# Kernel tuning notes

Measured on AMD Instinct MI355X. Metric: run time of the kernel, lower is better.

The kernel has to match this reference:

```python
import jax, jax.numpy as jnp
import numpy as np

N_NODES = 100000
N_EDGES = 1000000
NHID = 128
N_CLASSES = 5000


def setup_inputs() -> dict:
    key = jax.random.key(0)
    ks = jax.random.split(key, 8)
    feature = jax.random.normal(ks[0], (N_NODES, NHID), dtype=jnp.float32)
    # Linear weights stored as [in, out] so forward is x @ W + b
    W1 = jax.random.normal(ks[1], (2 * NHID, NHID), dtype=jnp.float32) * (1.0 / np.sqrt(2 * NHID))
    b1 = jnp.zeros((NHID,), dtype=jnp.float32)
    alpha = jnp.full((NHID,), 0.25, dtype=jnp.float32)  # PReLU per-channel init
    W2 = jax.random.normal(ks[2], (NHID, 2), dtype=jnp.float32) * (1.0 / np.sqrt(NHID))
    b2 = jnp.zeros((2,), dtype=jnp.float32)
    row = jax.random.randint(ks[3], (N_EDGES,), 0, N_NODES, dtype=jnp.int64)
    col = jax.random.randint(ks[4], (N_EDGES,), 0, N_NODES, dtype=jnp.int64)
    label = jax.random.randint(ks[5], (N_NODES,), 0, N_CLASSES, dtype=jnp.int64)
    return {"feature": feature, "W1": W1, "b1": b1, "alpha": alpha,
            "W2": W2, "b2": b2, "row": row, "col": col, "label": label}


def reference(feature, W1, b1, alpha, W2, b2, row, col, label):
    # per-edge label: 1 if endpoints share a cluster label
    y = (label[row] == label[col]).astype(jnp.int32)  # [E]
    # edge gather + concat: [E, 2*nhid]
    x = jnp.concatenate([feature[row], feature[col]], axis=1)
    h = x @ W1 + b1                                   # [E, nhid]
    h = jnp.where(h >= 0, h, alpha * h)               # PReLU, per-channel alpha
    logits = h @ W2 + b2                              # [E, 2]
    logp = jax.nn.log_softmax(logits, axis=-1)
    # mean cross-entropy over edges
    loss = -jnp.mean(jnp.take_along_axis(logp, y[:, None], axis=1))
    return loss
```

## Files before the change

### kernel.cpp

```cpp
#include <hip/hip_runtime.h>
#include <hip/hip_bf16.h>

typedef __bf16 bf16_t;
typedef bf16_t bf16x8 __attribute__((ext_vector_type(8)));
typedef float floatx4 __attribute__((ext_vector_type(4)));
typedef float floatx2 __attribute__((ext_vector_type(2)));

#define N_NODES 100000
#define N_EDGES 1000000
#define N_TILES 6250


__global__ __launch_bounds__(256) void k_prep(const float* __restrict__ W1,
                                              const float* __restrict__ b1,
                                              const float* __restrict__ alpha,
                                              const float* __restrict__ W2,
                                              const float* __restrict__ b2,
                                              bf16_t* __restrict__ WT,
                                              float* __restrict__ wabsp,
                                              float* __restrict__ u1g,
                                              float* __restrict__ u2g,
                                              float* __restrict__ constg,
                                              float* __restrict__ out) {
    __shared__ float w1L[128];
    int i = blockIdx.x * 256 + threadIdx.x;
    if (i < 32768) {
        int n = i >> 7;
        int k = i & 127;
        float v = (n < 128) ? W1[k * 128 + n] : W1[(k + 128) * 128 + (n - 128)];
        WT[i] = (bf16_t)v;
    }
    if (blockIdx.x == 128) {
        int t = threadIdx.x;
        if (t < 128) {
            float wd = W2[2 * t + 1] - W2[2 * t];
            float al = alpha[t];
            w1L[t] = wd * (1.f + al) * 0.5f;
            int c = (t & 7) * 16 + (t >> 3);
            float wdc = W2[2 * c + 1] - W2[2 * c];
            wabsp[t] = wdc * (1.f - alpha[c]) * 0.5f;
        }
        __syncthreads();
        if (t < 128) {
            float a1 = 0.f, a2 = 0.f;
            for (int j = 0; j < 128; ++j) {
                a1 = fmaf(W1[t * 128 + j], w1L[j], a1);
                a2 = fmaf(W1[(t + 128) * 128 + j], w1L[j], a2);
            }
            u1g[t] = a1;
            u2g[t] = a2;
        }
        if (t == 128) {
            float c = 0.f;
            for (int j = 0; j < 128; ++j) c = fmaf(w1L[j], b1[j], c);
            *constg = c + (b2[1] - b2[0]);
        }
        if (t == 129) out[0] = 0.f;
    }
}

__global__ __launch_bounds__(256) void k_gemm(const float* __restrict__ F,
                                              const bf16_t* __restrict__ WT,
                                              const float* __restrict__ b1,
                                              const float* __restrict__ u1g,
                                              const float* __restrict__ u2g,
                                              const int* __restrict__ label,
                                              unsigned char* __restrict__ PQ8,
                                              float4* __restrict__ aux_g) {
    const int w = threadIdx.x >> 6, lane = threadIdx.x & 63;
    const int l15 = lane & 15, quad = lane >> 4;
    const int h = w >> 1, jb = (w & 1) * 4;

    bf16x8 Bf[4][4];
    const bf16_t* wbase = WT + (size_t)(w * 64 + l15) * 128 + quad * 8;
#pragma unroll
    for (int s = 0; s < 4; ++s)
#pragma unroll
        for (int nt = 0; nt < 4; ++nt)
            Bf[s][nt] = *(const bf16x8*)(wbase + (size_t)nt * 2048 + s * 32);

    float bv[4];
#pragma unroll
    for (int nt = 0; nt < 4; ++nt)
        bv[nt] = (h == 0) ? b1[(jb + nt) * 16 + l15] : 0.f;

    for (int tile = blockIdx.x; tile < N_TILES; tile += gridDim.x) {
        const int m0 = tile * 16;
        const float4* Ar = (const float4*)(F + (size_t)(m0 + l15) * 128 + quad * 8);
        float4 fa[4], fb[4];
#pragma unroll
        for (int s = 0; s < 4; ++s) { fa[s] = Ar[s * 8]; fb[s] = Ar[s * 8 + 1]; }

        bf16x8 Af[4];
#pragma unroll
        for (int s = 0; s < 4; ++s) {
            bf16x8 v;
            v[0] = (bf16_t)fa[s].x; v[1] = (bf16_t)fa[s].y;
            v[2] = (bf16_t)fa[s].z; v[3] = (bf16_t)fa[s].w;
            v[4] = (bf16_t)fb[s].x; v[5] = (bf16_t)fb[s].y;
            v[6] = (bf16_t)fb[s].z; v[7] = (bf16_t)fb[s].w;
            Af[s] = v;
        }

        floatx4 acc[4] = {};
#pragma unroll
        for (int s = 0; s < 4; ++s)
#pragma unroll
            for (int nt = 0; nt < 4; ++nt)
                acc[nt] = __builtin_amdgcn_mfma_f32_16x16x32_bf16(Af[s], Bf[s][nt], acc[nt], 0, 0, 0);

        if (w == 0) {
            float s1 = 0.f, s2 = 0.f;
#pragma unroll
            for (int s = 0; s < 4; ++s) {
                const float* u1p = u1g + s * 32 + quad * 8;
                const float* u2p = u2g + s * 32 + quad * 8;
                float fv[8] = {fa[s].x, fa[s].y, fa[s].z, fa[s].w,
                               fb[s].x, fb[s].y, fb[s].z, fb[s].w};
#pragma unroll
                for (int j = 0; j < 8; ++j) {
                    s1 = fmaf(fv[j], u1p[j], s1);
                    s2 = fmaf(fv[j], u2p[j], s2);
                }
            }
            s1 += __shfl_xor(s1, 16, 64); s1 += __shfl_xor(s1, 32, 64);
            s2 += __shfl_xor(s2, 16, 64); s2 += __shfl_xor(s2, 32, 64);
            if (quad == 0) {
                int grow = m0 + l15;
                float4 av = {s1, s2, __int_as_float(label[grow]), 0.f};
                aux_g[grow] = av;
            }
        }

#pragma unroll
        for (int r = 0; r < 4; ++r) {
            int grow = m0 + quad * 4 + r;
            unsigned int pk = 0;
            pk = __builtin_amdgcn_cvt_pk_fp8_f32(acc[0][r] + bv[0], acc[1][r] + bv[1], pk, false);
            pk = __builtin_amdgcn_cvt_pk_fp8_f32(acc[2][r] + bv[2], acc[3][r] + bv[3], pk, true);
            *(unsigned int*)(PQ8 + (size_t)grow * 256 + h * 128 + l15 * 8 + jb) = pk;
        }
    }
}

__global__ __launch_bounds__(256) void k_edge_loss(const unsigned char* __restrict__ PQ8,
                                                   const float4* __restrict__ aux,
                                                   const float* __restrict__ wabsp,
                                                   const float* __restrict__ constg,
                                                   const int* __restrict__ row,
                                                   const int* __restrict__ col,
                                                   float* __restrict__ out) {
    const int lg = threadIdx.x & 15;
    const int group = (blockIdx.x * blockDim.x + threadIdx.x) >> 4;
    const int ng = (gridDim.x * blockDim.x) >> 4;
    const int ch = lg * 8;

    float wabs[8];
#pragma unroll
    for (int j = 0; j < 8; ++j) wabs[j] = wabsp[ch + j];
    const float CB = *constg;

    float acc = 0.f;
    for (int e = group; e < N_EDGES; e += 8 * ng) {
        int r[8], c[8];
#pragma unroll
        for (int k = 0; k < 8; ++k) {
            int ee = e + k * ng;
            int es = (ee < N_EDGES) ? ee : e;
            r[k] = row[es]; c[k] = col[es];
        }
        uint2 p[8], q[8];
#pragma unroll
        for (int k = 0; k < 8; ++k) {
            p[k] = *(const uint2*)(PQ8 + (size_t)r[k] * 256 + ch);
            q[k] = *(const uint2*)(PQ8 + (size_t)c[k] * 256 + 128 + ch);
        }
        int ee2 = e + (lg & 7) * ng;
        int es2 = (ee2 < N_EDGES) ? ee2 : e;
        const int* ibase = (lg < 8) ? row : col;
        float4 a = aux[ibase[es2]];

        float sab[8] = {0.f, 0.f, 0.f, 0.f, 0.f, 0.f, 0.f, 0.f};
#pragma unroll
        for (int k = 0; k < 8; ++k) {
            floatx2 p01 = __builtin_amdgcn_cvt_pk_f32_fp8((int)p[k].x, false);
            floatx2 p23 = __builtin_amdgcn_cvt_pk_f32_fp8((int)p[k].x, true);
            floatx2 p45 = __builtin_amdgcn_cvt_pk_f32_fp8((int)p[k].y, false);
            floatx2 p67 = __builtin_amdgcn_cvt_pk_f32_fp8((int)p[k].y, true);
            floatx2 q01 = __builtin_amdgcn_cvt_pk_f32_fp8((int)q[k].x, false);
            floatx2 q23 = __builtin_amdgcn_cvt_pk_f32_fp8((int)q[k].x, true);
            floatx2 q45 = __builtin_amdgcn_cvt_pk_f32_fp8((int)q[k].y, false);
            floatx2 q67 = __builtin_amdgcn_cvt_pk_f32_fp8((int)q[k].y, true);
            floatx2 h01 = p01 + q01;
            floatx2 h23 = p23 + q23;
            floatx2 h45 = p45 + q45;
            floatx2 h67 = p67 + q67;
            float s = sab[k];
            s = fmaf(fabsf(h01[0]), wabs[0], s);
            s = fmaf(fabsf(h01[1]), wabs[1], s);
            s = fmaf(fabsf(h23[0]), wabs[2], s);
            s = fmaf(fabsf(h23[1]), wabs[3], s);
            s = fmaf(fabsf(h45[0]), wabs[4], s);
            s = fmaf(fabsf(h45[1]), wabs[5], s);
            s = fmaf(fabsf(h67[0]), wabs[6], s);
            s = fmaf(fabsf(h67[1]), wabs[7], s);
            sab[k] = s;
        }
#pragma unroll
        for (int m = 8; m >= 1; m >>= 1) {
#pragma unroll
            for (int k = 0; k < 8; ++k) sab[k] += __shfl_xor(sab[k], m, 16);
        }
        float s2o = __shfl(a.y, (lg + 8) & 15, 16);
        float lzc = __shfl(a.z, (lg + 8) & 15, 16);
        float mysab = sab[0];
#pragma unroll
        for (int k = 1; k < 8; ++k) mysab = (lg == k) ? sab[k] : mysab;
        float D = a.x + s2o + CB + mysab;
        float sgn = (__float_as_int(a.z) == __float_as_int(lzc)) ? -D : D;
        float loss = fmaxf(sgn, 0.f) + __logf(1.f + __expf(-fabsf(sgn)));
        bool vld = (lg < 8) && (e + lg * ng < N_EDGES);
        acc += vld ? loss : 0.f;
    }
#pragma unroll
    for (int m = 32; m >= 1; m >>= 1) acc += __shfl_xor(acc, m, 64);
    __shared__ float sdata[4];
    int lane = threadIdx.x & 63;
    int wv = threadIdx.x >> 6;
    if (lane == 0) sdata[wv] = acc;
    __syncthreads();
    if (threadIdx.x == 0) {
        float s = (sdata[0] + sdata[1]) + (sdata[2] + sdata[3]);
        atomicAdd(out, s * (1.f / (float)N_EDGES));
    }
}

extern "C" void kernel_launch(void* const* d_in, const int* in_sizes, int n_in,
                              void* d_out, int out_size, void* d_ws, size_t ws_size,
                              hipStream_t stream) {
    const float* feature = (const float*)d_in[0];
    const float* W1      = (const float*)d_in[1];
    const float* b1      = (const float*)d_in[2];
    const float* alpha   = (const float*)d_in[3];
    const float* W2      = (const float*)d_in[4];
    const float* b2      = (const float*)d_in[5];
    const int*   row     = (const int*)d_in[6];
    const int*   col     = (const int*)d_in[7];
    const int*   label   = (const int*)d_in[8];
    float* out = (float*)d_out;

    char* ws = (char*)d_ws;
    unsigned char* PQ8 = (unsigned char*)(ws);
    float4* aux  = (float4*)(ws + 25600000);
    bf16_t* WT   = (bf16_t*)(ws + 27200000);
    float* wabsp = (float*)(ws + 27265536);
    float* u1g   = (float*)(ws + 27266048);
    float* u2g   = (float*)(ws + 27266560);
    float* constg= (float*)(ws + 27267072);

    k_prep<<<129, 256, 0, stream>>>(W1, b1, alpha, W2, b2, WT, wabsp, u1g, u2g,
                                    constg, out);
    k_gemm<<<1024, 256, 0, stream>>>(feature, WT, b1, u1g, u2g, label, PQ8, aux);
    k_edge_loss<<<4096, 256, 0, stream>>>(PQ8, aux, wabsp, constg, row, col, out);
}
```

Measured before the change: 209.5 us.

## Prefetch next feature tile in GEMM loop and parallelize prep reductions

Result: slower. 218.4 us (+4.2%).

```diff
diff --git a/kernel.cpp b/kernel.cpp
--- a/kernel.cpp
+++ b/kernel.cpp
@@ -22,40 +22,51 @@
                                               float* __restrict__ u2g,
                                               float* __restrict__ constg,
                                               float* __restrict__ out) {
-    __shared__ float w1L[128];
-    int i = blockIdx.x * 256 + threadIdx.x;
-    if (i < 32768) {
+    const int t = threadIdx.x;
+    if (blockIdx.x < 128) {
+        int i = blockIdx.x * 256 + t;
         int n = i >> 7;
         int k = i & 127;
         float v = (n < 128) ? W1[k * 128 + n] : W1[(k + 128) * 128 + (n - 128)];
         WT[i] = (bf16_t)v;
-    }
-    if (blockIdx.x == 128) {
-        int t = threadIdx.x;
-        if (t < 128) {
-            float wd = W2[2 * t + 1] - W2[2 * t];
-            float al = alpha[t];
-            w1L[t] = wd * (1.f + al) * 0.5f;
-            int c = (t & 7) * 16 + (t >> 3);
-            float wdc = W2[2 * c + 1] - W2[2 * c];
-            wabsp[t] = wdc * (1.f - alpha[c]) * 0.5f;
-        }
-        __syncthreads();
-        if (t < 128) {
-            float a1 = 0.f, a2 = 0.f;
-            for (int j = 0; j < 128; ++j) {
-                a1 = fmaf(W1[t * 128 + j], w1L[j], a1);
-                a2 = fmaf(W1[(t + 128) * 128 + j], w1L[j], a2);
-            }
-            u1g[t] = a1;
-            u2g[t] = a2;
-        }
-        if (t == 128) {
-            float c = 0.f;
-            for (int j = 0; j < 128; ++j) c = fmaf(w1L[j], b1[j], c);
-            *constg = c + (b2[1] - b2[0]);
-        }
-        if (t == 129) out[0] = 0.f;
+        return;
+    }
+    __shared__ float w1L[128];
+    __shared__ float part1[256];
+    __shared__ float part2[256];
+    if (t < 128) {
+        float wd = W2[2 * t + 1] - W2[2 * t];
+        float al = alpha[t];
+        w1L[t] = wd * (1.f + al) * 0.5f;
+        int c = (t & 7) * 16 + (t >> 3);
+        float wdc = W2[2 * c + 1] - W2[2 * c];
+        wabsp[t] = wdc * (1.f - alpha[c]) * 0.5f;
+    }
+    __syncthreads();
+    {
+        int o = t >> 1, hf = t & 1;
+        const float* r1 = W1 + (size_t)o * 128 + hf * 64;
+        const float* r2 = W1 + (size_t)(o + 128) * 128 + hf * 64;
+        const float* wl = w1L + hf * 64;
+        float a1 = 0.f, a2 = 0.f;
+#pragma unroll 8
+        for (int j = 0; j < 64; ++j) {
+            a1 = fmaf(r1[j], wl[j], a1);
+            a2 = fmaf(r2[j], wl[j], a2);
+        }
+        part1[t] = a1;
+        part2[t] = a2;
+    }
+    __syncthreads();
+    if (t < 128) {
+        u1g[t] = part1[2 * t] + part1[2 * t + 1];
+        u2g[t] = part2[2 * t] + part2[2 * t + 1];
+    }
+    if (t < 64) {
+        float c = fmaf(w1L[t], b1[t], w1L[t + 64] * b1[t + 64]);
+#pragma unroll
+        for (int m = 32; m >= 1; m >>= 1) c += __shfl_xor(c, m, 64);
+        if (t == 0) { *constg = c + (b2[1] - b2[0]); out[0] = 0.f; }
     }
 }
 
@@ -84,12 +95,17 @@
     for (int nt = 0; nt < 4; ++nt)
         bv[nt] = (h == 0) ? b1[(jb + nt) * 16 + l15] : 0.f;
 
-    for (int tile = blockIdx.x; tile < N_TILES; tile += gridDim.x) {
+    int tile = blockIdx.x;
+    float4 fa[4], fb[4];
+    if (tile < N_TILES) {
+        const float4* Ar = (const float4*)(F + (size_t)(tile * 16 + l15) * 128 + quad * 8);
+#pragma unroll
+        for (int s = 0; s < 4; ++s) { fa[s] = Ar[s * 8]; fb[s] = Ar[s * 8 + 1]; }
+    }
+
+    while (tile < N_TILES) {
+        const int next = tile + gridDim.x;
         const int m0 = tile * 16;
-        const float4* Ar = (const float4*)(F + (size_t)(m0 + l15) * 128 + quad * 8);
-        float4 fa[4], fb[4];
-#pragma unroll
-        for (int s = 0; s < 4; ++s) { fa[s] = Ar[s * 8]; fb[s] = Ar[s * 8 + 1]; }
 
         bf16x8 Af[4];
 #pragma unroll
@@ -101,13 +117,11 @@
             v[6] = (bf16_t)fb[s].z; v[7] = (bf16_t)fb[s].w;
             Af[s] = v;
         }
-
-        floatx4 acc[4] = {};
-#pragma unroll
-        for (int s = 0; s < 4; ++s)
-#pragma unroll
-            for (int nt = 0; nt < 4; ++nt)
-                acc[nt] = __builtin_amdgcn_mfma_f32_16x16x32_bf16(Af[s], Bf[s][nt], acc[nt], 0, 0, 0);
+        if (next < N_TILES) {
+            const float4* Ar = (const float4*)(F + (size_t)(next * 16 + l15) * 128 + quad * 8);
+#pragma unroll
+            for (int s = 0; s < 4; ++s) { fa[s] = Ar[s * 8]; fb[s] = Ar[s * 8 + 1]; }
+        }
 
         if (w == 0) {
             float s1 = 0.f, s2 = 0.f;
@@ -115,12 +129,12 @@
             for (int s = 0; s < 4; ++s) {
                 const float* u1p = u1g + s * 32 + quad * 8;
                 const float* u2p = u2g + s * 32 + quad * 8;
-                float fv[8] = {fa[s].x, fa[s].y, fa[s].z, fa[s].w,
-                               fb[s].x, fb[s].y, fb[s].z, fb[s].w};
+                bf16x8 aw = Af[s];
 #pragma unroll
                 for (int j = 0; j < 8; ++j) {
-                    s1 = fmaf(fv[j], u1p[j], s1);
-                    s2 = fmaf(fv[j], u2p[j], s2);
+                    float fv = (float)aw[j];
+                    s1 = fmaf(fv, u1p[j], s1);
+                    s2 = fmaf(fv, u2p[j], s2);
                 }
             }
             s1 += __shfl_xor(s1, 16, 64); s1 += __shfl_xor(s1, 32, 64);
@@ -132,6 +146,13 @@
             }
         }
 
+        floatx4 acc[4] = {};
+#pragma unroll
+        for (int s = 0; s < 4; ++s)
+#pragma unroll
+            for (int nt = 0; nt < 4; ++nt)
+                acc[nt] = __builtin_amdgcn_mfma_f32_16x16x32_bf16(Af[s], Bf[s][nt], acc[nt], 0, 0, 0);
+
 #pragma unroll
         for (int r = 0; r < 4; ++r) {
             int grow = m0 + quad * 4 + r;
@@ -140,6 +161,7 @@
             pk = __builtin_amdgcn_cvt_pk_fp8_f32(acc[2][r] + bv[2], acc[3][r] + bv[3], pk, true);
             *(unsigned int*)(PQ8 + (size_t)grow * 256 + h * 128 + l15 * 8 + jb) = pk;
         }
+        tile = next;
     }
 }
 
```
